# Performance work log

Measured on AMD Instinct MI355X. Metric: run time of the kernel, lower is better.

The kernel has to match this reference:

```python
import jax, jax.numpy as jnp
import numpy as np

N, E, H, R, L, G = 50000, 800000, 128, 128, 3, 64
CUTOFF = 5.0
EDGE_IN = 2 * H + R + 1  # 385


def setup_inputs() -> dict:
    key = jax.random.key(0)
    ks = jax.random.split(key, 20)
    s = 0.05
    inp = {
        "x": jax.random.randint(ks[0], (N,), 0, 100),
        "edge_index": jax.random.randint(ks[1], (2, E), 0, N),
        "edge_weight": jax.random.uniform(ks[2], (E,), jnp.float32) * CUTOFF,
        "edge_attr": jax.random.uniform(ks[3], (E, R), jnp.float32),
        "batch": jnp.sort(jax.random.randint(ks[4], (N,), 0, G)),
        "emb": jax.random.normal(ks[5], (100, H), jnp.float32) * s,
        "ew1": jax.random.normal(ks[6], (L, EDGE_IN, H), jnp.float32) * s,
        "eb1": jnp.zeros((L, H), jnp.float32),
        "ew2": jax.random.normal(ks[7], (L, H, H), jnp.float32) * s,
        "eb2": jnp.zeros((L, H), jnp.float32),
        "nw1": jax.random.normal(ks[8], (L, 2 * H, H), jnp.float32) * s,
        "nb1": jnp.zeros((L, H), jnp.float32),
        "nw2": jax.random.normal(ks[9], (L, H, H), jnp.float32) * s,
        "nb2": jnp.zeros((L, H), jnp.float32),
        "linw": jax.random.normal(ks[10], (H, H), jnp.float32) * s,
        "linb": jnp.zeros((H,), jnp.float32),
    }
    return inp


def reference(x, edge_index, edge_weight, edge_attr, batch,
              emb, ew1, eb1, ew2, eb2, nw1, nb1, nw2, nb2, linw, linb):
    h = emb[x]  # [N, H]
    row, col = edge_index[0], edge_index[1]
    d_raw = (edge_weight / CUTOFF)[:, None]  # [E, 1]
    n_layers = ew1.shape[0]
    for l in range(n_layers):
        # edge MLP: gather endpoints, concat with edge feats + scaled distance
        edge_in = jnp.concatenate([h[row], h[col], edge_attr, d_raw], axis=-1)  # [E, 2H+R+1]
        m = jax.nn.silu(edge_in @ ew1[l] + eb1[l])
        m = jax.nn.silu(m @ ew2[l] + eb2[l])  # [E, H]
        # scatter-add messages to source nodes (index_add_ on row)
        agg = jax.ops.segment_sum(m, row, num_segments=h.shape[0])  # [N, H]
        # node MLP + residual
        node_in = jnp.concatenate([h, agg], axis=-1)  # [N, 2H]
        upd = jax.nn.silu(node_in @ nw1[l] + nb1[l]) @ nw2[l] + nb2[l]
        h = h + upd
    # global mean pool per graph
    sums = jax.ops.segment_sum(h, batch, num_segments=G)  # [G, H]
    cnt = jax.ops.segment_sum(jnp.ones((h.shape[0], 1), h.dtype), batch, num_segments=G)
    pooled = sums / jnp.maximum(cnt, 1.0)
    return jax.nn.relu(pooled) @ linw + linb  # [G, H]
```

## Files before the change

kernel.cpp:

```cpp
#include <hip/hip_runtime.h>

#define N_NODES 50000
#define N_EDGES 800000
#define HD      128
#define NG      64
#define NLAYER  3
#define INV_CUTOFF 0.2f

__device__ __forceinline__ float silu_f(float x) {
    return x / (1.0f + __expf(-x));
}

__global__ __launch_bounds__(256) void embed_kernel(
    const int* __restrict__ x, const float* __restrict__ emb,
    float* __restrict__ h)
{
    int i = blockIdx.x * 256 + threadIdx.x;
    int n = i >> 5;
    int q = (i & 31) << 2;
    *(float4*)&h[(size_t)n * HD + q] =
        *(const float4*)&emb[(size_t)x[n] * HD + q];
}


#define YS_STORE(JB)                                                          \
    _Pragma("unroll")                                                         \
    for (int jj = 0; jj < 4; ++jj) {                                          \
        int kl = (u << 2) + jj;                                               \
        *(float4*)&Ys[kl * HD + ((trq ^ u) << 2)] =                           \
            make_float4(acc[0][(JB)+jj], acc[1][(JB)+jj],                     \
                        acc[2][(JB)+jj], acc[3][(JB)+jj]);                    \
        *(float4*)&Ys[kl * HD + (((trq + 1) ^ u) << 2)] =                     \
            make_float4(acc[4][(JB)+jj], acc[5][(JB)+jj],                     \
                        acc[6][(JB)+jj], acc[7][(JB)+jj]);                    \
    }

__global__ __launch_bounds__(256, 2) void edge_kernel(
    const float* __restrict__ h, const int* __restrict__ ei,
    const float* __restrict__ ew, const float* __restrict__ ea,
    const float* __restrict__ W1, const float* __restrict__ b1,
    const float* __restrict__ W2, const float* __restrict__ b2,
    float* __restrict__ agg)
{
    __shared__ float Ws[32 * HD];
    __shared__ float As[32 * HD];
    __shared__ float Ys[32 * HD];
    __shared__ int   srow[128], scol[128];
    __shared__ float sd[128];

    const int tid = threadIdx.x;
    const int e0  = blockIdx.x * 128;

    if (tid < 128) {
        int e = e0 + tid;
        srow[tid] = ei[e];
        scol[tid] = ei[N_EDGES + e];
        sd[tid]   = ew[e] * INV_CUTOFF;
    }
    __syncthreads();

    const int t15 = tid & 15;
    const int tcL = t15 << 2;
    const int tr  = (tid >> 4) << 3;
    const int trq = tr >> 2;
    const int t7  = tid & 7;
    const int t8  = tid >> 3;
    const int kq  = t7 << 2;

    int eA[4], rA[4], cA[4], csA[4];
#pragma unroll
    for (int i = 0; i < 4; ++i) {
        eA[i]  = t8 + (i << 5);
        rA[i]  = srow[eA[i]];
        cA[i]  = scol[eA[i]];
        csA[i] = (((eA[i] >> 2) ^ t7) << 2) | (eA[i] & 3);
    }

    float4 wreg[4], areg[4];

    float acc[8][8];
#pragma unroll
    for (int i = 0; i < 8; ++i)
#pragma unroll
        for (int j = 0; j < 8; ++j) acc[i][j] = 0.0f;

#pragma unroll
    for (int i = 0; i < 4; ++i) {
        int flat = tid + (i << 8);
        wreg[i] = *(const float4*)&W1[(size_t)(flat >> 5) * HD + ((flat & 31) << 2)];
        areg[i] = *(const float4*)&h[(size_t)rA[i] * HD + kq];
    }

#pragma unroll 1
    for (int ch = 0; ch < 12; ++ch) {
        if (ch) __syncthreads();
#pragma unroll
        for (int i = 0; i < 4; ++i) {
            int flat = tid + (i << 8);
            *(float4*)&Ws[(flat >> 5) * HD + ((flat & 31) << 2)] = wreg[i];
        }
#pragma unroll
        for (int i = 0; i < 4; ++i) {
            float4 v = areg[i];
            As[(kq + 0) * HD + csA[i]] = v.x;
            As[(kq + 1) * HD + csA[i]] = v.y;
            As[(kq + 2) * HD + csA[i]] = v.z;
            As[(kq + 3) * HD + csA[i]] = v.w;
        }
        __syncthreads();
        if (ch < 11) {
            int cn = ch + 1;
#pragma unroll
            for (int i = 0; i < 4; ++i) {
                int flat = tid + (i << 8);
                wreg[i] = *(const float4*)&W1[
                    (size_t)((cn << 5) + (flat >> 5)) * HD + ((flat & 31) << 2)];
                const float* src;
                if (cn < 4)      src = h  + (size_t)rA[i] * HD + (cn << 5) + kq;
                else if (cn < 8) src = h  + (size_t)cA[i] * HD + ((cn - 4) << 5) + kq;
                else             src = ea + (size_t)(e0 + eA[i]) * HD + ((cn - 8) << 5) + kq;
                areg[i] = *(const float4*)src;
            }
        }
#pragma unroll 8
        for (int k = 0; k < 32; ++k) {
            int s = (k >> 2) & 7;
            float a[8], b[8];
            *(float4*)&a[0] = *(float4*)&As[k * HD + ((trq ^ s) << 2)];
            *(float4*)&a[4] = *(float4*)&As[k * HD + (((trq + 1) ^ s) << 2)];
            *(float4*)&b[0] = *(float4*)&Ws[k * HD + tcL];
            *(float4*)&b[4] = *(float4*)&Ws[k * HD + tcL + 64];
#pragma unroll
            for (int i = 0; i < 8; ++i)
#pragma unroll
                for (int j = 0; j < 8; ++j)
                    acc[i][j] = fmaf(a[i], b[j], acc[i][j]);
        }
    }

    {
        float bb[8], wd[8];
        *(float4*)&bb[0] = *(const float4*)&b1[tcL];
        *(float4*)&bb[4] = *(const float4*)&b1[tcL + 64];
        *(float4*)&wd[0] = *(const float4*)&W1[(size_t)384 * HD + tcL];
        *(float4*)&wd[4] = *(const float4*)&W1[(size_t)384 * HD + tcL + 64];
#pragma unroll
        for (int i = 0; i < 8; ++i) {
            float d = sd[tr + i];
#pragma unroll
            for (int j = 0; j < 8; ++j)
                acc[i][j] = silu_f(acc[i][j] + bb[j] + d * wd[j]);
        }
    }
    __syncthreads();

    float acc2[8][8];
#pragma unroll
    for (int i = 0; i < 8; ++i)
#pragma unroll
        for (int j = 0; j < 8; ++j) acc2[i][j] = 0.0f;

#pragma unroll
    for (int i = 0; i < 4; ++i) {
        int flat = tid + (i << 8);
        wreg[i] = *(const float4*)&W2[(size_t)(flat >> 5) * HD + ((flat & 31) << 2)];
    }

#pragma unroll 1
    for (int p = 0; p < 4; ++p) {
        int sel = (p < 2) ? p : (p - 2);
        if ((t15 >> 3) == sel) {
            const int u = t15 & 7;
            if (p < 2) { YS_STORE(0) } else { YS_STORE(4) }
        }
#pragma unroll
        for (int i = 0; i < 4; ++i) {
            int flat = tid + (i << 8);
            *(float4*)&Ws[(flat >> 5) * HD + ((flat & 31) << 2)] = wreg[i];
        }
        __syncthreads();
        if (p < 3) {
#pragma unroll
            for (int i = 0; i < 4; ++i) {
                int flat = tid + (i << 8);
                wreg[i] = *(const float4*)&W2[
                    (size_t)(((p + 1) << 5) + (flat >> 5)) * HD + ((flat & 31) << 2)];
            }
        }
#pragma unroll 8
        for (int k = 0; k < 32; ++k) {
            int s = (k >> 2) & 7;
            float a[8], b[8];
            *(float4*)&a[0] = *(float4*)&Ys[k * HD + ((trq ^ s) << 2)];
            *(float4*)&a[4] = *(float4*)&Ys[k * HD + (((trq + 1) ^ s) << 2)];
            *(float4*)&b[0] = *(float4*)&Ws[k * HD + tcL];
            *(float4*)&b[4] = *(float4*)&Ws[k * HD + tcL + 64];
#pragma unroll
            for (int i = 0; i < 8; ++i)
#pragma unroll
                for (int j = 0; j < 8; ++j)
                    acc2[i][j] = fmaf(a[i], b[j], acc2[i][j]);
        }
        __syncthreads();
    }

    {
        float bb[8];
        *(float4*)&bb[0] = *(const float4*)&b2[tcL];
        *(float4*)&bb[4] = *(const float4*)&b2[tcL + 64];
#pragma unroll
        for (int i = 0; i < 8; ++i) {
            float* dst = agg + (size_t)srow[tr + i] * HD;
#pragma unroll
            for (int j = 0; j < 4; ++j)
                unsafeAtomicAdd(&dst[tcL + j], silu_f(acc2[i][j] + bb[j]));
#pragma unroll
            for (int j = 0; j < 4; ++j)
                unsafeAtomicAdd(&dst[tcL + 64 + j], silu_f(acc2[i][4 + j] + bb[4 + j]));
        }
    }
}

__global__ __launch_bounds__(256, 2) void node_kernel(
    float* __restrict__ h, const float* __restrict__ agg,
    const float* __restrict__ W1, const float* __restrict__ b1,
    const float* __restrict__ W2, const float* __restrict__ b2)
{
    __shared__ float Ws[32 * HD];
    __shared__ float As[32 * HD];
    __shared__ float Ys[32 * HD];

    const int tid = threadIdx.x;
    const int n0  = blockIdx.x * 128;

    const int t15 = tid & 15;
    const int tcL = t15 << 2;
    const int tr  = (tid >> 4) << 3;
    const int trq = tr >> 2;
    const int t7  = tid & 7;
    const int t8  = tid >> 3;
    const int kq  = t7 << 2;

    int nA[4], csA[4];
#pragma unroll
    for (int i = 0; i < 4; ++i) {
        int e = t8 + (i << 5);
        int n = n0 + e;
        nA[i]  = n < N_NODES ? n : (N_NODES - 1);
        csA[i] = (((e >> 2) ^ t7) << 2) | (e & 3);
    }

    float4 wreg[4], areg[4];

    float acc[8][8];
#pragma unroll
    for (int i = 0; i < 8; ++i)
#pragma unroll
        for (int j = 0; j < 8; ++j) acc[i][j] = 0.0f;

#pragma unroll
    for (int i = 0; i < 4; ++i) {
        int flat = tid + (i << 8);
        wreg[i] = *(const float4*)&W1[(size_t)(flat >> 5) * HD + ((flat & 31) << 2)];
        areg[i] = *(const float4*)&h[(size_t)nA[i] * HD + kq];
    }

#pragma unroll 1
    for (int ch = 0; ch < 8; ++ch) {
        if (ch) __syncthreads();
#pragma unroll
        for (int i = 0; i < 4; ++i) {
            int flat = tid + (i << 8);
            *(float4*)&Ws[(flat >> 5) * HD + ((flat & 31) << 2)] = wreg[i];
        }
#pragma unroll
        for (int i = 0; i < 4; ++i) {
            float4 v = areg[i];
            As[(kq + 0) * HD + csA[i]] = v.x;
            As[(kq + 1) * HD + csA[i]] = v.y;
            As[(kq + 2) * HD + csA[i]] = v.z;
            As[(kq + 3) * HD + csA[i]] = v.w;
        }
        __syncthreads();
        if (ch < 7) {
            int cn = ch + 1;
#pragma unroll
            for (int i = 0; i < 4; ++i) {
                int flat = tid + (i << 8);
                wreg[i] = *(const float4*)&W1[
                    (size_t)((cn << 5) + (flat >> 5)) * HD + ((flat & 31) << 2)];
                const float* src = (cn < 4)
                    ? h   + (size_t)nA[i] * HD + (cn << 5) + kq
                    : agg + (size_t)nA[i] * HD + ((cn - 4) << 5) + kq;
                areg[i] = *(const float4*)src;
            }
        }
#pragma unroll 8
        for (int k = 0; k < 32; ++k) {
            int s = (k >> 2) & 7;
            float a[8], b[8];
            *(float4*)&a[0] = *(float4*)&As[k * HD + ((trq ^ s) << 2)];
            *(float4*)&a[4] = *(float4*)&As[k * HD + (((trq + 1) ^ s) << 2)];
            *(float4*)&b[0] = *(float4*)&Ws[k * HD + tcL];
            *(float4*)&b[4] = *(float4*)&Ws[k * HD + tcL + 64];
#pragma unroll
            for (int i = 0; i < 8; ++i)
#pragma unroll
                for (int j = 0; j < 8; ++j)
                    acc[i][j] = fmaf(a[i], b[j], acc[i][j]);
        }
    }

    {
        float bb[8];
        *(float4*)&bb[0] = *(const float4*)&b1[tcL];
        *(float4*)&bb[4] = *(const float4*)&b1[tcL + 64];
#pragma unroll
        for (int i = 0; i < 8; ++i)
#pragma unroll
            for (int j = 0; j < 8; ++j)
                acc[i][j] = silu_f(acc[i][j] + bb[j]);
    }
    __syncthreads();

    float acc2[8][8];
#pragma unroll
    for (int i = 0; i < 8; ++i)
#pragma unroll
        for (int j = 0; j < 8; ++j) acc2[i][j] = 0.0f;

#pragma unroll
    for (int i = 0; i < 4; ++i) {
        int flat = tid + (i << 8);
        wreg[i] = *(const float4*)&W2[(size_t)(flat >> 5) * HD + ((flat & 31) << 2)];
    }

#pragma unroll 1
    for (int p = 0; p < 4; ++p) {
        int sel = (p < 2) ? p : (p - 2);
        if ((t15 >> 3) == sel) {
            const int u = t15 & 7;
            if (p < 2) { YS_STORE(0) } else { YS_STORE(4) }
        }
#pragma unroll
        for (int i = 0; i < 4; ++i) {
            int flat = tid + (i << 8);
            *(float4*)&Ws[(flat >> 5) * HD + ((flat & 31) << 2)] = wreg[i];
        }
        __syncthreads();
        if (p < 3) {
#pragma unroll
            for (int i = 0; i < 4; ++i) {
                int flat = tid + (i << 8);
                wreg[i] = *(const float4*)&W2[
                    (size_t)(((p + 1) << 5) + (flat >> 5)) * HD + ((flat & 31) << 2)];
            }
        }
#pragma unroll 8
        for (int k = 0; k < 32; ++k) {
            int s = (k >> 2) & 7;
            float a[8], b[8];
            *(float4*)&a[0] = *(float4*)&Ys[k * HD + ((trq ^ s) << 2)];
            *(float4*)&a[4] = *(float4*)&Ys[k * HD + (((trq + 1) ^ s) << 2)];
            *(float4*)&b[0] = *(float4*)&Ws[k * HD + tcL];
            *(float4*)&b[4] = *(float4*)&Ws[k * HD + tcL + 64];
#pragma unroll
            for (int i = 0; i < 8; ++i)
#pragma unroll
                for (int j = 0; j < 8; ++j)
                    acc2[i][j] = fmaf(a[i], b[j], acc2[i][j]);
        }
        __syncthreads();
    }

    {
        float bb[8];
        *(float4*)&bb[0] = *(const float4*)&b2[tcL];
        *(float4*)&bb[4] = *(const float4*)&b2[tcL + 64];
#pragma unroll
        for (int i = 0; i < 8; ++i) {
            int n = n0 + tr + i;
            if (n < N_NODES) {
                float* dst = h + (size_t)n * HD;
                float4 o0 = *(float4*)&dst[tcL];
                float4 o1 = *(float4*)&dst[tcL + 64];
                o0.x += acc2[i][0] + bb[0];
                o0.y += acc2[i][1] + bb[1];
                o0.z += acc2[i][2] + bb[2];
                o0.w += acc2[i][3] + bb[3];
                o1.x += acc2[i][4] + bb[4];
                o1.y += acc2[i][5] + bb[5];
                o1.z += acc2[i][6] + bb[6];
                o1.w += acc2[i][7] + bb[7];
                *(float4*)&dst[tcL]      = o0;
                *(float4*)&dst[tcL + 64] = o1;
            }
        }
    }
}

__global__ __launch_bounds__(256) void pool_kernel(
    const float* __restrict__ h, const int* __restrict__ batch,
    const float* __restrict__ linw, const float* __restrict__ linb,
    float* __restrict__ out)
{
    const int g   = blockIdx.x;
    const int tid = threadIdx.x;

    int lo = 0, hi = N_NODES;
    while (lo < hi) { int mid = (lo + hi) >> 1; if (batch[mid] < g) lo = mid + 1; else hi = mid; }
    int s_lo = lo;
    lo = s_lo; hi = N_NODES;
    while (lo < hi) { int mid = (lo + hi) >> 1; if (batch[mid] < g + 1) lo = mid + 1; else hi = mid; }
    int s_hi = lo;

    const int col  = tid & 127;
    const int half = tid >> 7;
    float s = 0.0f;
    for (int r = s_lo + half; r < s_hi; r += 2)
        s += h[(size_t)r * HD + col];

    __shared__ float tmp[2][HD];
    __shared__ float pool[HD];
    tmp[half][col] = s;
    __syncthreads();
    if (tid < HD) {
        float cnt = (float)(s_hi - s_lo);
        cnt = fmaxf(cnt, 1.0f);
        float v = (tmp[0][tid] + tmp[1][tid]) / cnt;
        pool[tid] = fmaxf(v, 0.0f);
    }
    __syncthreads();
    if (tid < HD) {
        float a = linb[tid];
        for (int k = 0; k < HD; ++k)
            a = fmaf(pool[k], linw[k * HD + tid], a);
        out[(size_t)g * HD + tid] = a;
    }
}

extern "C" void kernel_launch(void* const* d_in, const int* in_sizes, int n_in,
                              void* d_out, int out_size, void* d_ws, size_t ws_size,
                              hipStream_t stream)
{
    const int*   x     = (const int*)  d_in[0];
    const int*   ei    = (const int*)  d_in[1];
    const float* ew    = (const float*)d_in[2];
    const float* ea    = (const float*)d_in[3];
    const int*   batch = (const int*)  d_in[4];
    const float* emb   = (const float*)d_in[5];
    const float* ew1   = (const float*)d_in[6];
    const float* eb1   = (const float*)d_in[7];
    const float* ew2   = (const float*)d_in[8];
    const float* eb2   = (const float*)d_in[9];
    const float* nw1   = (const float*)d_in[10];
    const float* nb1   = (const float*)d_in[11];
    const float* nw2   = (const float*)d_in[12];
    const float* nb2   = (const float*)d_in[13];
    const float* linw  = (const float*)d_in[14];
    const float* linb  = (const float*)d_in[15];
    float*       out   = (float*)d_out;

    float* h   = (float*)d_ws;
    float* agg = h + (size_t)N_NODES * HD;

    embed_kernel<<<(N_NODES * (HD / 4)) / 256, 256, 0, stream>>>(x, emb, h);

    for (int l = 0; l < NLAYER; ++l) {
        hipMemsetAsync(agg, 0, (size_t)N_NODES * HD * sizeof(float), stream);
        edge_kernel<<<N_EDGES / 128, 256, 0, stream>>>(
            h, ei, ew, ea,
            ew1 + (size_t)l * 385 * HD, eb1 + (size_t)l * HD,
            ew2 + (size_t)l * HD * HD,  eb2 + (size_t)l * HD, agg);
        node_kernel<<<(N_NODES + 127) / 128, 256, 0, stream>>>(
            h, agg,
            nw1 + (size_t)l * 256 * HD, nb1 + (size_t)l * HD,
            nw2 + (size_t)l * HD * HD,  nb2 + (size_t)l * HD);
    }

    pool_kernel<<<NG, 256, 0, stream>>>(h, batch, linw, linb, out);
}
```

Before: 6.957 ms.

## Sort edges by source row, pre-reduce messages, remap blocks across XCDs

Builds a counting-sort permutation of edges by source node (histogram, single-block scan, scatter) once per call, and makes the edge kernel process edges in sorted order. Each thread sums consecutive messages that share a row before issuing atomics, which cuts atomic traffic and improves locality of h[row] gathers. Block indices are remapped so contiguous edge chunks land on the same XCD, and occupancy hints rise from 2 to 3 blocks per CU for both MLP kernels. The cost is added preprocessing kernels, including a serial single-block scan, plus edge_attr reads that are now scattered rather than streamed. Register pressure may also rise under the tighter occupancy bound.

```diff
diff --git a/kernel.cpp b/kernel.cpp
--- a/kernel.cpp
+++ b/kernel.cpp
@@ -9,6 +9,50 @@
 
 __device__ __forceinline__ float silu_f(float x) {
     return x / (1.0f + __expf(-x));
+}
+
+__global__ __launch_bounds__(256) void hist_kernel(
+    const int* __restrict__ ei, int* __restrict__ cnt)
+{
+    int e = blockIdx.x * 256 + threadIdx.x;
+    if (e < N_EDGES) atomicAdd(&cnt[ei[e]], 1);
+}
+
+__global__ __launch_bounds__(1024) void scan_kernel(int* __restrict__ cnt)
+{
+    __shared__ int buf[1024];
+    __shared__ int carry_s;
+    const int tid = threadIdx.x;
+    if (tid == 0) carry_s = 0;
+    __syncthreads();
+    for (int base = 0; base < N_NODES; base += 1024) {
+        int idx = base + tid;
+        int v = (idx < N_NODES) ? cnt[idx] : 0;
+        buf[tid] = v;
+        __syncthreads();
+        for (int off = 1; off < 1024; off <<= 1) {
+            int t = (tid >= off) ? buf[tid - off] : 0;
+            __syncthreads();
+            buf[tid] += t;
+            __syncthreads();
+        }
+        int incl  = buf[tid];
+        int carry = carry_s;
+        __syncthreads();
+        if (idx < N_NODES) cnt[idx] = carry + incl - v;
+        if (tid == 1023) carry_s = carry + buf[1023];
+        __syncthreads();
+    }
+}
+
+__global__ __launch_bounds__(256) void scatter_kernel(
+    const int* __restrict__ ei, int* __restrict__ cnt, int* __restrict__ perm)
+{
+    int e = blockIdx.x * 256 + threadIdx.x;
+    if (e < N_EDGES) {
+        int p = atomicAdd(&cnt[ei[e]], 1);
+        perm[p] = e;
+    }
 }
 
 __global__ __launch_bounds__(256) void embed_kernel(
@@ -35,9 +79,10 @@
                         acc[6][(JB)+jj], acc[7][(JB)+jj]);                    \
     }
 
-__global__ __launch_bounds__(256, 2) void edge_kernel(
+__global__ __launch_bounds__(256, 3) void edge_kernel(
     const float* __restrict__ h, const int* __restrict__ ei,
     const float* __restrict__ ew, const float* __restrict__ ea,
+    const int* __restrict__ perm,
     const float* __restrict__ W1, const float* __restrict__ b1,
     const float* __restrict__ W2, const float* __restrict__ b2,
     float* __restrict__ agg)
@@ -45,14 +90,20 @@
     __shared__ float Ws[32 * HD];
     __shared__ float As[32 * HD];
     __shared__ float Ys[32 * HD];
-    __shared__ int   srow[128], scol[128];
+    __shared__ int   srow[128], scol[128], sper[128];
     __shared__ float sd[128];
 
     const int tid = threadIdx.x;
-    const int e0  = blockIdx.x * 128;
+
+    const int nwg = N_EDGES / 128;
+    const int q8  = nwg >> 3, r8 = nwg & 7;
+    int xcd = blockIdx.x & 7, sub = blockIdx.x >> 3;
+    int bid = (xcd < r8 ? xcd * (q8 + 1) : r8 * (q8 + 1) + (xcd - r8) * q8) + sub;
+    const int e0 = bid * 128;
 
     if (tid < 128) {
-        int e = e0 + tid;
+        int e = perm[e0 + tid];
+        sper[tid] = e;
         srow[tid] = ei[e];
         scol[tid] = ei[N_EDGES + e];
         sd[tid]   = ew[e] * INV_CUTOFF;
@@ -67,12 +118,13 @@
     const int t8  = tid >> 3;
     const int kq  = t7 << 2;
 
-    int eA[4], rA[4], cA[4], csA[4];
+    int eA[4], rA[4], cA[4], csA[4], eO[4];
 #pragma unroll
     for (int i = 0; i < 4; ++i) {
         eA[i]  = t8 + (i << 5);
         rA[i]  = srow[eA[i]];
         cA[i]  = scol[eA[i]];
+        eO[i]  = sper[eA[i]];
         csA[i] = (((eA[i] >> 2) ^ t7) << 2) | (eA[i] & 3);
     }
 
@@ -118,7 +170,7 @@
                 const float* src;
                 if (cn < 4)      src = h  + (size_t)rA[i] * HD + (cn << 5) + kq;
                 else if (cn < 8) src = h  + (size_t)cA[i] * HD + ((cn - 4) << 5) + kq;
-                else             src = ea + (size_t)(e0 + eA[i]) * HD + ((cn - 8) << 5) + kq;
+                else             src = ea + (size_t)eO[i] * HD + ((cn - 8) << 5) + kq;
                 areg[i] = *(const float4*)src;
             }
         }
@@ -208,20 +260,40 @@
         float bb[8];
         *(float4*)&bb[0] = *(const float4*)&b2[tcL];
         *(float4*)&bb[4] = *(const float4*)&b2[tcL + 64];
-#pragma unroll
-        for (int i = 0; i < 8; ++i) {
-            float* dst = agg + (size_t)srow[tr + i] * HD;
-#pragma unroll
-            for (int j = 0; j < 4; ++j)
-                unsafeAtomicAdd(&dst[tcL + j], silu_f(acc2[i][j] + bb[j]));
-#pragma unroll
-            for (int j = 0; j < 4; ++j)
-                unsafeAtomicAdd(&dst[tcL + 64 + j], silu_f(acc2[i][4 + j] + bb[4 + j]));
-        }
-    }
-}
-
-__global__ __launch_bounds__(256, 2) void node_kernel(
+        float sum[8];
+        int cur_row = srow[tr];
+#pragma unroll
+        for (int j = 0; j < 8; ++j) sum[j] = silu_f(acc2[0][j] + bb[j]);
+#pragma unroll
+        for (int i = 1; i < 8; ++i) {
+            int rr = srow[tr + i];
+            if (rr != cur_row) {
+                float* dst = agg + (size_t)cur_row * HD;
+#pragma unroll
+                for (int j = 0; j < 4; ++j)
+                    unsafeAtomicAdd(&dst[tcL + j], sum[j]);
+#pragma unroll
+                for (int j = 0; j < 4; ++j)
+                    unsafeAtomicAdd(&dst[tcL + 64 + j], sum[4 + j]);
+                cur_row = rr;
+#pragma unroll
+                for (int j = 0; j < 8; ++j) sum[j] = silu_f(acc2[i][j] + bb[j]);
+            } else {
+#pragma unroll
+                for (int j = 0; j < 8; ++j) sum[j] += silu_f(acc2[i][j] + bb[j]);
+            }
+        }
+        float* dst = agg + (size_t)cur_row * HD;
+#pragma unroll
+        for (int j = 0; j < 4; ++j)
+            unsafeAtomicAdd(&dst[tcL + j], sum[j]);
+#pragma unroll
+        for (int j = 0; j < 4; ++j)
+            unsafeAtomicAdd(&dst[tcL + 64 + j], sum[4 + j]);
+    }
+}
+
+__global__ __launch_bounds__(256, 3) void node_kernel(
     float* __restrict__ h, const float* __restrict__ agg,
     const float* __restrict__ W1, const float* __restrict__ b1,
     const float* __restrict__ W2, const float* __restrict__ b2)
@@ -461,15 +533,22 @@
     const float* linb  = (const float*)d_in[15];
     float*       out   = (float*)d_out;
 
-    float* h   = (float*)d_ws;
-    float* agg = h + (size_t)N_NODES * HD;
+    float* h    = (float*)d_ws;
+    float* agg  = h + (size_t)N_NODES * HD;
+    int*   perm = (int*)(agg + (size_t)N_NODES * HD);
+    int*   cnt  = perm + N_EDGES;
+
+    hipMemsetAsync(cnt, 0, (size_t)N_NODES * sizeof(int), stream);
+    hist_kernel<<<(N_EDGES + 255) / 256, 256, 0, stream>>>(ei, cnt);
+    scan_kernel<<<1, 1024, 0, stream>>>(cnt);
+    scatter_kernel<<<(N_EDGES + 255) / 256, 256, 0, stream>>>(ei, cnt, perm);
 
     embed_kernel<<<(N_NODES * (HD / 4)) / 256, 256, 0, stream>>>(x, emb, h);
 
     for (int l = 0; l < NLAYER; ++l) {
         hipMemsetAsync(agg, 0, (size_t)N_NODES * HD * sizeof(float), stream);
         edge_kernel<<<N_EDGES / 128, 256, 0, stream>>>(
-            h, ei, ew, ea,
+            h, ei, ew, ea, perm,
             ew1 + (size_t)l * 385 * HD, eb1 + (size_t)l * HD,
             ew2 + (size_t)l * HD * HD,  eb2 + (size_t)l * HD, agg);
         node_kernel<<<(N_NODES + 127) / 128, 256, 0, stream>>>(
```

Measured after the change: 5.774 ms. 17.0% less time.
